# Optimization experiments

Measured on AMD Instinct MI355X. Metric: run time of the kernel, lower is better.

The kernel has to match this reference:

```python
import jax, jax.numpy as jnp
import numpy as np

NUM_NODES = 500000
INPUT_DIM = 256
ATTN_DIM = 64
NUM_GRAPHS = 512


def setup_inputs() -> dict:
    key = jax.random.key(0)
    ks = jax.random.split(key, 6)
    x = jax.random.normal(ks[0], (NUM_NODES, INPUT_DIM), dtype=jnp.float32)
    batch = jnp.sort(jax.random.randint(ks[1], (NUM_NODES,), 0, NUM_GRAPHS, dtype=jnp.int32)).astype(jnp.int64)
    # Xavier-uniform style init for linear weights, normal(0, 0.1) for context
    lim1 = float(np.sqrt(6.0 / (INPUT_DIM + ATTN_DIM)))
    W_att = jax.random.uniform(ks[2], (ATTN_DIM, INPUT_DIM), minval=-lim1, maxval=lim1, dtype=jnp.float32)
    b_att = jnp.zeros((ATTN_DIM,), dtype=jnp.float32)
    ctx = 0.1 * jax.random.normal(ks[3], (ATTN_DIM,), dtype=jnp.float32)
    lim2 = float(np.sqrt(6.0 / (INPUT_DIM + INPUT_DIM)))
    W_out = jax.random.uniform(ks[4], (INPUT_DIM, INPUT_DIM), minval=-lim2, maxval=lim2, dtype=jnp.float32)
    b_out = jnp.zeros((INPUT_DIM,), dtype=jnp.float32)
    return {"x": x, "batch": batch, "W_att": W_att, "b_att": b_att, "ctx": ctx, "W_out": W_out, "b_out": b_out}


def reference(x, batch, W_att, b_att, ctx, W_out, b_out):
    seg = batch.astype(jnp.int32)
    # attention scores per node: tanh(x W^T + b) . ctx  -> [N]
    logits = jnp.tanh(x @ W_att.T + b_att)
    scores = logits @ ctx  # [N]
    # segment-wise stable softmax
    seg_max = jax.ops.segment_max(scores, seg, num_segments=NUM_GRAPHS)
    exp_s = jnp.exp(scores - seg_max[seg])
    seg_sum = jax.ops.segment_sum(exp_s, seg, num_segments=NUM_GRAPHS)
    w = exp_s / (seg_sum[seg] + 1e-8)  # [N]
    # weighted segment-sum pooling -> [B, D]
    pooled = jax.ops.segment_sum(x * w[:, None], seg, num_segments=NUM_GRAPHS)
    return pooled @ W_out.T + b_out
```

## Files before the change

### kernel.cpp

```cpp
#include <hip/hip_runtime.h>
#include <hip/hip_bf16.h>
#include <math.h>

#define N_NODES 500000
#define DIM 256
#define ADIM 64
#define NG 512
#define NBLK 7813

typedef __attribute__((ext_vector_type(8))) short short8;
typedef __attribute__((ext_vector_type(4))) float floatx4;

__device__ inline unsigned short f2bf(float f) {
    union { float f; unsigned int u; } v; v.f = f;
    unsigned int u = v.u;
    unsigned int r = u + 0x7FFFu + ((u >> 16) & 1u);
    return (unsigned short)(r >> 16);
}

__device__ inline unsigned pk_bf2(float a, float b) {
    __hip_bfloat162 h = __float22bfloat162_rn(make_float2(a, b));
    union { __hip_bfloat162 h; unsigned u; } cv; cv.h = h;
    return cv.u;
}

__device__ inline float tanh_fast(float xv) {
    float e = __expf(2.0f * fabsf(xv));
    float r = 1.0f - 2.0f * __builtin_amdgcn_rcpf(e + 1.0f);
    return copysignf(r, xv);
}

__global__ __launch_bounds__(256) void k_prep(const float* __restrict__ W_out,
                                              const float* __restrict__ W_att,
                                              const float* __restrict__ ctx,
                                              float* __restrict__ Wt_out,
                                              unsigned short* __restrict__ Wbf,
                                              float* __restrict__ cnorm,
                                              float* __restrict__ zero_base) {
    int b = blockIdx.x, t = threadIdx.x;
    if (b < 256) {
        int idx = b * 256 + t;
        int o = idx >> 8, d = idx & 255;
        Wt_out[d * DIM + o] = W_out[idx];
    } else if (b < 320) {
        int idx = (b - 256) * 256 + t;
        Wbf[idx] = f2bf(W_att[idx]);
    } else if (b < 834) {
        int idx = (b - 320) * 256 + t;
        zero_base[idx] = 0.f;
    } else if (t == 0) {
        float s = 0.f;
        for (int k = 0; k < ADIM; ++k) s += fabsf(ctx[k]);
        *cnorm = s;
    }
}

__global__ __launch_bounds__(256, 3) void k_fused(const float* __restrict__ x,
                                                  const unsigned short* __restrict__ Wbf,
                                                  const float* __restrict__ b_att,
                                                  const float* __restrict__ ctx,
                                                  const int* __restrict__ batch,
                                                  const float* __restrict__ cnorm,
                                                  float* __restrict__ accum,
                                                  float* __restrict__ ssum) {
    __shared__ __align__(16) unsigned short xs[8][65][40];
    __shared__ float sacc[4][64];
    __shared__ float pbuf[64];
    __shared__ int   gbuf[64];
    __shared__ __align__(16) float redp[4][64][4];

    const int t = threadIdx.x;
    const int wave = t >> 6;
    const int lane = t & 63;
    const int quad = lane >> 4;
    const int lcol = lane & 15;
    const int base = blockIdx.x * 64;
    const float cn = *cnorm;

    short8 bfrag[8];
    {
        const unsigned short* wr = Wbf + (size_t)(16 * wave + lcol) * DIM + quad * 8;
#pragma unroll
        for (int s = 0; s < 8; ++s) bfrag[s] = *(const short8*)(wr + s * 32);
    }

    const int srow = t >> 2;
    const int sk = (t & 3) * 4;
    const int node_s = base + srow;
    const bool valid = node_s < N_NODES;
    const float* xrow = x + (size_t)node_s * DIM;

    float4 h0[8], h1[8];
#pragma unroll
    for (int s = 0; s < 8; ++s) { h0[s] = make_float4(0.f, 0.f, 0.f, 0.f); h1[s] = h0[s]; }
    if (valid) {
#pragma unroll
        for (int s = 0; s < 8; ++s) {
            h0[s] = *(const float4*)(xrow + s * 32 + sk);
            h1[s] = *(const float4*)(xrow + s * 32 + sk + 16);
        }
    }
#pragma unroll
    for (int s = 0; s < 8; ++s) {
        uint2 w0, w1;
        w0.x = pk_bf2(h0[s].x, h0[s].y); w0.y = pk_bf2(h0[s].z, h0[s].w);
        w1.x = pk_bf2(h1[s].x, h1[s].y); w1.y = pk_bf2(h1[s].z, h1[s].w);
        *(uint2*)&xs[s][srow][sk]      = w0;
        *(uint2*)&xs[s][srow][sk + 16] = w1;
    }
    __syncthreads();

    floatx4 acc[4];
#pragma unroll
    for (int mt = 0; mt < 4; ++mt) acc[mt] = (floatx4)0.f;
#pragma unroll
    for (int s = 0; s < 8; ++s) {
#pragma unroll
        for (int mt = 0; mt < 4; ++mt) {
            short8 afrag = *(const short8*)&xs[s][mt * 16 + lcol][quad * 8];
            acc[mt] = __builtin_amdgcn_mfma_f32_16x16x32_bf16(afrag, bfrag[s], acc[mt], 0, 0, 0);
        }
    }

    const float ctxv = ctx[16 * wave + lcol];
    const float bv = b_att[16 * wave + lcol];
#pragma unroll
    for (int mt = 0; mt < 4; ++mt) {
#pragma unroll
        for (int r = 0; r < 4; ++r) {
            float v = ctxv * tanh_fast(acc[mt][r] + bv);
            v += __shfl_xor(v, 1);
            v += __shfl_xor(v, 2);
            v += __shfl_xor(v, 4);
            v += __shfl_xor(v, 8);
            if (lcol == 0) sacc[wave][mt * 16 + quad * 4 + r] = v;
        }
    }
    __syncthreads();
    if (t < 64) {
        float sres = (sacc[0][t] + sacc[1][t]) + (sacc[2][t] + sacc[3][t]);
        int node = base + t;
        bool v = node < N_NODES;
        pbuf[t] = v ? __expf(sres - cn) : 0.f;
        gbuf[t] = batch[v ? node : (N_NODES - 1)];
    }
    __syncthreads();

    const int g0 = gbuf[0];
    const int g1 = gbuf[63];
    const int ps = lane >> 3;
    const int pc = (lane & 7) * 4;
    for (int g = g0; g <= g1; ++g) {
        float4 a4 = make_float4(0.f, 0.f, 0.f, 0.f);
#pragma unroll 4
        for (int j = 0; j < 16; ++j) {
            int i = (wave << 4) + j;
            float wp = (gbuf[i] == g) ? pbuf[i] : 0.f;
            if (wp != 0.f) {
                uint2 v = *(const uint2*)&xs[ps][i][pc];
                a4.x += wp * __uint_as_float(v.x << 16);
                a4.y += wp * __uint_as_float(v.x & 0xffff0000u);
                a4.z += wp * __uint_as_float(v.y << 16);
                a4.w += wp * __uint_as_float(v.y & 0xffff0000u);
            }
        }
        *(float4*)&redp[wave][lane][0] = a4;
        float sp = 0.f;
        if (t < 64) sp = (gbuf[t] == g) ? pbuf[t] : 0.f;
        __syncthreads();
        float r = ((redp[0][t >> 2][t & 3] + redp[1][t >> 2][t & 3]) +
                   (redp[2][t >> 2][t & 3] + redp[3][t >> 2][t & 3]));
        atomicAdd(&accum[(size_t)g * DIM + t], r);
        if (t < 64) {
            sp += __shfl_xor(sp, 1);  sp += __shfl_xor(sp, 2);
            sp += __shfl_xor(sp, 4);  sp += __shfl_xor(sp, 8);
            sp += __shfl_xor(sp, 16); sp += __shfl_xor(sp, 32);
            if (t == 0) atomicAdd(&ssum[g], sp);
        }
        __syncthreads();
    }
}

__global__ __launch_bounds__(256) void k_out(const float* __restrict__ accum,
                                             const float* __restrict__ ssum,
                                             const float* __restrict__ WtOut,
                                             const float* __restrict__ b_out,
                                             float* __restrict__ out) {
    int g = blockIdx.x;
    int t = threadIdx.x;
    __shared__ float pl[256];
    float inv = 1.0f / (ssum[g] + 1e-20f);
    pl[t] = accum[(size_t)g * DIM + t] * inv;
    __syncthreads();
    float acc = b_out[t];
#pragma unroll 4
    for (int d = 0; d < DIM; ++d) acc += pl[d] * WtOut[d * DIM + t];
    out[(size_t)g * DIM + t] = acc;
}

extern "C" void kernel_launch(void* const* d_in, const int* in_sizes, int n_in,
                              void* d_out, int out_size, void* d_ws, size_t ws_size,
                              hipStream_t stream) {
    (void)in_sizes; (void)n_in; (void)out_size; (void)ws_size;
    const float* x     = (const float*)d_in[0];
    const int*   batch = (const int*)d_in[1];
    const float* W_att = (const float*)d_in[2];
    const float* b_att = (const float*)d_in[3];
    const float* ctx   = (const float*)d_in[4];
    const float* W_out = (const float*)d_in[5];
    const float* b_out = (const float*)d_in[6];
    float* out = (float*)d_out;

    float* accum = (float*)d_ws;
    float* ssum  = accum + 131072;
    float* Wt    = ssum + 512;
    unsigned short* Wbf = (unsigned short*)(Wt + 65536);
    float* cnorm = (float*)(Wbf + 16384);

    k_prep<<<dim3(835), dim3(256), 0, stream>>>(W_out, W_att, ctx, Wt, Wbf, cnorm, accum);
    k_fused<<<dim3(NBLK), dim3(256), 0, stream>>>(x, Wbf, b_att, ctx, batch, cnorm, accum, ssum);
    k_out<<<dim3(NG), dim3(256), 0, stream>>>(accum, ssum, Wt, b_out, out);
}
```

Measured before the change: 698.0 us.

## Make fused pooling kernel persistent with double-buffered tiles and carried segment accumulators

Replaces the one-block-per-64-nodes launch with a persistent grid of 768 blocks, each walking a contiguous range of 32-node tiles. The next tile's x rows are prefetched into registers and written to a second LDS buffer while the current tile is processed. Per-graph partial sums stay in registers across tiles and are flushed with atomics only when the graph id changes, which cuts global atomic traffic. The cost is more barriers per node and a serial dependency chain inside each block, and fewer tiles in flight may lower achieved memory bandwidth.

```diff
diff --git a/kernel.cpp b/kernel.cpp
--- a/kernel.cpp
+++ b/kernel.cpp
@@ -6,10 +6,14 @@
 #define DIM 256
 #define ADIM 64
 #define NG 512
-#define NBLK 7813
+#define TILE 32
+#define NTILES 15625
+#define GRID_F 768
 
 typedef __attribute__((ext_vector_type(8))) short short8;
 typedef __attribute__((ext_vector_type(4))) float floatx4;
+
+#define BAR() asm volatile("s_waitcnt lgkmcnt(0)\n\ts_barrier" ::: "memory")
 
 __device__ inline unsigned short f2bf(float f) {
     union { float f; unsigned int u; } v; v.f = f;
@@ -63,19 +67,23 @@
                                                   const float* __restrict__ cnorm,
                                                   float* __restrict__ accum,
                                                   float* __restrict__ ssum) {
-    __shared__ __align__(16) unsigned short xs[8][65][40];
-    __shared__ float sacc[4][64];
-    __shared__ float pbuf[64];
-    __shared__ int   gbuf[64];
-    __shared__ __align__(16) float redp[4][64][4];
+    __shared__ __align__(16) unsigned short xs[2][8][33][40];
+    __shared__ float sacc[4][32];
+    __shared__ float pbuf[32];
+    __shared__ int   gbuf[32];
+    __shared__ __align__(16) float redp[4][DIM];
 
     const int t = threadIdx.x;
     const int wave = t >> 6;
     const int lane = t & 63;
     const int quad = lane >> 4;
     const int lcol = lane & 15;
-    const int base = blockIdx.x * 64;
     const float cn = *cnorm;
+
+    const int b = blockIdx.x;
+    const int q = NTILES / GRID_F, r = NTILES % GRID_F;
+    const int t0 = b * q + min(b, r);
+    const int t1 = t0 + q + (b < r ? 1 : 0);
 
     short8 bfrag[8];
     {
@@ -84,101 +92,127 @@
         for (int s = 0; s < 8; ++s) bfrag[s] = *(const short8*)(wr + s * 32);
     }
 
-    const int srow = t >> 2;
-    const int sk = (t & 3) * 4;
-    const int node_s = base + srow;
-    const bool valid = node_s < N_NODES;
-    const float* xrow = x + (size_t)node_s * DIM;
-
-    float4 h0[8], h1[8];
-#pragma unroll
-    for (int s = 0; s < 8; ++s) { h0[s] = make_float4(0.f, 0.f, 0.f, 0.f); h1[s] = h0[s]; }
-    if (valid) {
-#pragma unroll
-        for (int s = 0; s < 8; ++s) {
-            h0[s] = *(const float4*)(xrow + s * 32 + sk);
-            h1[s] = *(const float4*)(xrow + s * 32 + sk + 16);
-        }
-    }
-#pragma unroll
-    for (int s = 0; s < 8; ++s) {
-        uint2 w0, w1;
-        w0.x = pk_bf2(h0[s].x, h0[s].y); w0.y = pk_bf2(h0[s].z, h0[s].w);
-        w1.x = pk_bf2(h1[s].x, h1[s].y); w1.y = pk_bf2(h1[s].z, h1[s].w);
-        *(uint2*)&xs[s][srow][sk]      = w0;
-        *(uint2*)&xs[s][srow][sk + 16] = w1;
-    }
-    __syncthreads();
-
-    floatx4 acc[4];
-#pragma unroll
-    for (int mt = 0; mt < 4; ++mt) acc[mt] = (floatx4)0.f;
-#pragma unroll
-    for (int s = 0; s < 8; ++s) {
-#pragma unroll
-        for (int mt = 0; mt < 4; ++mt) {
-            short8 afrag = *(const short8*)&xs[s][mt * 16 + lcol][quad * 8];
-            acc[mt] = __builtin_amdgcn_mfma_f32_16x16x32_bf16(afrag, bfrag[s], acc[mt], 0, 0, 0);
-        }
-    }
+    const int srow = t >> 3;
+    const int soff = (t & 7) * 4;
+    const int ps = lane >> 3;
+    const int pc = (lane & 7) * 4;
 
     const float ctxv = ctx[16 * wave + lcol];
     const float bv = b_att[16 * wave + lcol];
-#pragma unroll
-    for (int mt = 0; mt < 4; ++mt) {
-#pragma unroll
-        for (int r = 0; r < 4; ++r) {
-            float v = ctxv * tanh_fast(acc[mt][r] + bv);
-            v += __shfl_xor(v, 1);
-            v += __shfl_xor(v, 2);
-            v += __shfl_xor(v, 4);
-            v += __shfl_xor(v, 8);
-            if (lcol == 0) sacc[wave][mt * 16 + quad * 4 + r] = v;
-        }
-    }
-    __syncthreads();
-    if (t < 64) {
-        float sres = (sacc[0][t] + sacc[1][t]) + (sacc[2][t] + sacc[3][t]);
-        int node = base + t;
-        bool v = node < N_NODES;
-        pbuf[t] = v ? __expf(sres - cn) : 0.f;
-        gbuf[t] = batch[v ? node : (N_NODES - 1)];
-    }
-    __syncthreads();
-
-    const int g0 = gbuf[0];
-    const int g1 = gbuf[63];
-    const int ps = lane >> 3;
-    const int pc = (lane & 7) * 4;
-    for (int g = g0; g <= g1; ++g) {
-        float4 a4 = make_float4(0.f, 0.f, 0.f, 0.f);
-#pragma unroll 4
-        for (int j = 0; j < 16; ++j) {
-            int i = (wave << 4) + j;
-            float wp = (gbuf[i] == g) ? pbuf[i] : 0.f;
-            if (wp != 0.f) {
-                uint2 v = *(const uint2*)&xs[ps][i][pc];
-                a4.x += wp * __uint_as_float(v.x << 16);
-                a4.y += wp * __uint_as_float(v.x & 0xffff0000u);
-                a4.z += wp * __uint_as_float(v.y << 16);
-                a4.w += wp * __uint_as_float(v.y & 0xffff0000u);
-            }
-        }
-        *(float4*)&redp[wave][lane][0] = a4;
-        float sp = 0.f;
-        if (t < 64) sp = (gbuf[t] == g) ? pbuf[t] : 0.f;
-        __syncthreads();
-        float r = ((redp[0][t >> 2][t & 3] + redp[1][t >> 2][t & 3]) +
-                   (redp[2][t >> 2][t & 3] + redp[3][t >> 2][t & 3]));
-        atomicAdd(&accum[(size_t)g * DIM + t], r);
+
+    float4 a4 = make_float4(0.f, 0.f, 0.f, 0.f);
+    float s_acc = 0.f;
+    int cur_g = -1;
+    int cur = 0;
+
+    auto FLUSH = [&](int gf) {
+        *(float4*)&redp[wave][(lane >> 3) * 32 + (lane & 7) * 4] = a4;
+        BAR();
+        float rsum = (redp[0][t] + redp[1][t]) + (redp[2][t] + redp[3][t]);
+        atomicAdd(&accum[(size_t)gf * DIM + t], rsum);
         if (t < 64) {
+            float sp = (t < 32) ? s_acc : 0.f;
             sp += __shfl_xor(sp, 1);  sp += __shfl_xor(sp, 2);
             sp += __shfl_xor(sp, 4);  sp += __shfl_xor(sp, 8);
-            sp += __shfl_xor(sp, 16); sp += __shfl_xor(sp, 32);
-            if (t == 0) atomicAdd(&ssum[g], sp);
-        }
-        __syncthreads();
-    }
+            sp += __shfl_xor(sp, 16);
+            if (t == 0) atomicAdd(&ssum[gf], sp);
+        }
+        BAR();
+    };
+
+    {
+        const float* xrow = x + (size_t)(t0 * TILE + srow) * DIM + soff;
+        float4 h0[8];
+#pragma unroll
+        for (int s = 0; s < 8; ++s) h0[s] = *(const float4*)(xrow + s * 32);
+#pragma unroll
+        for (int s = 0; s < 8; ++s) {
+            uint2 w;
+            w.x = pk_bf2(h0[s].x, h0[s].y);
+            w.y = pk_bf2(h0[s].z, h0[s].w);
+            *(uint2*)&xs[0][s][srow][soff] = w;
+        }
+        BAR();
+    }
+
+    float4 h[8];
+    for (int ti = t0; ti < t1; ++ti) {
+        const bool haveNext = (ti + 1 < t1);
+        if (haveNext) {
+            const float* xrow = x + (size_t)((ti + 1) * TILE + srow) * DIM + soff;
+#pragma unroll
+            for (int s = 0; s < 8; ++s) h[s] = *(const float4*)(xrow + s * 32);
+        }
+        const int bval = batch[ti * TILE + (t & 31)];
+
+        floatx4 acc[2];
+        acc[0] = (floatx4)0.f; acc[1] = (floatx4)0.f;
+#pragma unroll
+        for (int s = 0; s < 8; ++s) {
+#pragma unroll
+            for (int mt = 0; mt < 2; ++mt) {
+                short8 afrag = *(const short8*)&xs[cur][s][mt * 16 + lcol][quad * 8];
+                acc[mt] = __builtin_amdgcn_mfma_f32_16x16x32_bf16(afrag, bfrag[s], acc[mt], 0, 0, 0);
+            }
+        }
+
+#pragma unroll
+        for (int mt = 0; mt < 2; ++mt) {
+#pragma unroll
+            for (int r4 = 0; r4 < 4; ++r4) {
+                float v = ctxv * tanh_fast(acc[mt][r4] + bv);
+                v += __shfl_xor(v, 1);
+                v += __shfl_xor(v, 2);
+                v += __shfl_xor(v, 4);
+                v += __shfl_xor(v, 8);
+                if (lcol == 0) sacc[wave][mt * 16 + quad * 4 + r4] = v;
+            }
+        }
+        BAR();
+
+        if (t < 32) {
+            float sres = (sacc[0][t] + sacc[1][t]) + (sacc[2][t] + sacc[3][t]);
+            pbuf[t] = __expf(sres - cn);
+            gbuf[t] = bval;
+        }
+        if (haveNext) {
+#pragma unroll
+            for (int s = 0; s < 8; ++s) {
+                uint2 w;
+                w.x = pk_bf2(h[s].x, h[s].y);
+                w.y = pk_bf2(h[s].z, h[s].w);
+                *(uint2*)&xs[cur ^ 1][s][srow][soff] = w;
+            }
+        }
+        BAR();
+
+        const int g0 = gbuf[0];
+        const int g1 = gbuf[31];
+        if (cur_g < 0) cur_g = g0;
+        for (int g = cur_g; g <= g1; ++g) {
+#pragma unroll
+            for (int j = 0; j < 8; ++j) {
+                int i = (wave << 3) + j;
+                float wp = (gbuf[i] == g) ? pbuf[i] : 0.f;
+                if (wp != 0.f) {
+                    uint2 v = *(const uint2*)&xs[cur][ps][i][pc];
+                    a4.x += wp * __uint_as_float(v.x << 16);
+                    a4.y += wp * __uint_as_float(v.x & 0xffff0000u);
+                    a4.z += wp * __uint_as_float(v.y << 16);
+                    a4.w += wp * __uint_as_float(v.y & 0xffff0000u);
+                }
+            }
+            if (t < 32) s_acc += (gbuf[t] == g) ? pbuf[t] : 0.f;
+            if (g < g1) {
+                FLUSH(g);
+                a4 = make_float4(0.f, 0.f, 0.f, 0.f);
+                s_acc = 0.f;
+            }
+        }
+        cur_g = g1;
+        cur ^= 1;
+    }
+    FLUSH(cur_g);
 }
 
 __global__ __launch_bounds__(256) void k_out(const float* __restrict__ accum,
@@ -218,6 +252,6 @@
     float* cnorm = (float*)(Wbf + 16384);
 
     k_prep<<<dim3(835), dim3(256), 0, stream>>>(W_out, W_att, ctx, Wt, Wbf, cnorm, accum);
-    k_fused<<<dim3(NBLK), dim3(256), 0, stream>>>(x, Wbf, b_att, ctx, batch, cnorm, accum, ssum);
+    k_fused<<<dim3(GRID_F), dim3(256), 0, stream>>>(x, Wbf, b_att, ctx, batch, cnorm, accum, ssum);
     k_out<<<dim3(NG), dim3(256), 0, stream>>>(accum, ssum, Wt, b_out, out);
 }
```

New measurement: 707.5 us. No clear change (+1.4%).
